# Kernel optimization log

Hardware: AMD Instinct MI355X
Metric: run time of the kernel (lower is better)

## Reference

```python
import jax, jax.numpy as jnp
import numpy as np

V, D, H_FF, NH, L = 32000, 1024, 4096, 16, 4
HD = D // NH  # 64
B, T = 2, 2048
EPS = 1e-6
ROPE_BASE = 10000.0


def setup_inputs() -> dict:
    key = jax.random.key(0)
    ks = jax.random.split(key, 16)
    s = 0.02
    inp = {
        "idx": jax.random.randint(ks[0], (B, T), 0, V, dtype=jnp.int32),
        "targets": jax.random.randint(ks[1], (B, T), 0, V, dtype=jnp.int32),
        "embed": jax.random.normal(ks[2], (V, D), jnp.float32) * s,
        "wq": jax.random.normal(ks[3], (L, D, D), jnp.float32) * s,
        "wk": jax.random.normal(ks[4], (L, D, D), jnp.float32) * s,
        "wv": jax.random.normal(ks[5], (L, D, D), jnp.float32) * s,
        "wo": jax.random.normal(ks[6], (L, D, D), jnp.float32) * s,
        "w_gate": jax.random.normal(ks[7], (L, D, H_FF), jnp.float32) * s,
        "w_up": jax.random.normal(ks[8], (L, D, H_FF), jnp.float32) * s,
        "w_down": jax.random.normal(ks[9], (L, H_FF, D), jnp.float32) * s,
        "attn_norm": jnp.ones((L, D), jnp.float32),
        "mlp_norm": jnp.ones((L, D), jnp.float32),
        "final_norm": jnp.ones((D,), jnp.float32),
        "lm_head": jax.random.normal(ks[10], (V, D), jnp.float32) * s,
    }
    return inp


def rms_norm(x, w):
    var = jnp.mean(jnp.square(x), axis=-1, keepdims=True)
    return x * jax.lax.rsqrt(var + EPS) * w


def make_rope(t_len, hd):
    inv_freq = 1.0 / (ROPE_BASE ** (jnp.arange(0, hd, 2, dtype=jnp.float32) / hd))
    angles = jnp.arange(t_len, dtype=jnp.float32)[:, None] * inv_freq[None, :]  # [T, HD/2]
    return jnp.cos(angles), jnp.sin(angles)


def apply_rope(x, cos, sin):
    # x: [B, T, NH, HD]; half-split rotation (HF Llama style)
    x1, x2 = jnp.split(x, 2, axis=-1)
    c = cos[None, :, None, :]
    s = sin[None, :, None, :]
    return jnp.concatenate([x1 * c - x2 * s, x2 * c + x1 * s], axis=-1)


def forward(idx, targets, embed, wq, wk, wv, wo, w_gate, w_up, w_down,
            attn_norm, mlp_norm, final_norm, lm_head):
    b, t_len = idx.shape
    x = embed[idx]  # [B, T, D]
    cos, sin = make_rope(t_len, HD)
    causal = jnp.tril(jnp.ones((t_len, t_len), dtype=bool))
    scale = 1.0 / np.sqrt(HD)
    for l in range(L):
        # attention
        h = rms_norm(x, attn_norm[l])
        q = (h @ wq[l]).reshape(b, t_len, NH, HD)
        k = (h @ wk[l]).reshape(b, t_len, NH, HD)
        v = (h @ wv[l]).reshape(b, t_len, NH, HD)
        q = apply_rope(q, cos, sin)
        k = apply_rope(k, cos, sin)
        scores = jnp.einsum('bqhd,bkhd->bhqk', q, k) * scale
        scores = jnp.where(causal[None, None], scores, -jnp.inf)
        attn = jax.nn.softmax(scores, axis=-1)
        o = jnp.einsum('bhqk,bkhd->bqhd', attn, v).reshape(b, t_len, D)
        x = x + o @ wo[l]
        # SwiGLU MLP
        h = rms_norm(x, mlp_norm[l])
        x = x + (jax.nn.silu(h @ w_gate[l]) * (h @ w_up[l])) @ w_down[l]
    x = rms_norm(x, final_norm)
    logits = jnp.einsum('btd,vd->btv', x, lm_head)  # [B, T, V]
    logp = jax.nn.log_softmax(logits, axis=-1)
    nll = -jnp.take_along_axis(logp, targets[..., None], axis=-1)[..., 0]
    loss = jnp.mean(nll)
    return logits, loss


def reference(idx, targets, embed, wq, wk, wv, wo, w_gate, w_up, w_down,
              attn_norm, mlp_norm, final_norm, lm_head):
    return forward(idx, targets, embed, wq, wk, wv, wo, w_gate, w_up, w_down,
                   attn_norm, mlp_norm, final_norm, lm_head)
```

## Files before the change

### kernel.cpp

```cpp
#include <hip/hip_runtime.h>

typedef __attribute__((ext_vector_type(8))) short short8;
typedef __attribute__((ext_vector_type(4))) float f32x4;
typedef __attribute__((ext_vector_type(8))) unsigned short u16x8;
typedef unsigned short u16;

#define V_SIZE 32000
#define D_MODEL 1024
#define HFF 4096
#define NHEAD 16
#define HDIM 64
#define NLAYER 4
#define BT 4096
#define TSEQ 2048
#define QKV_STRIDE 3072
#define GU_STRIDE 8192
#define QSCALE 0.18033688011112043f

__device__ __forceinline__ u16 f2bf(float f) {
  union { float f; unsigned u; } v; v.f = f;
  unsigned r = v.u + 0x7fffu + ((v.u >> 16) & 1u);
  return (u16)(r >> 16);
}
__device__ __forceinline__ float bf2f(u16 h) {
  union { unsigned u; float f; } v; v.u = ((unsigned)h) << 16;
  return v.f;
}

__device__ __forceinline__ void gload_lds16(const void* g, void* l) {
  __builtin_amdgcn_global_load_lds((__attribute__((address_space(1))) void*)g,
                                   (__attribute__((address_space(3))) void*)l, 16, 0, 0);
}


__global__ void rope_table_kernel(float* __restrict__ cosb, float* __restrict__ sinb) {
  int i = blockIdx.x * 256 + threadIdx.x;
  int t = i >> 5, fi = i & 31;
  float freq = exp2f(-(2.0f * (float)fi / 64.0f) * log2f(10000.0f));
  float ang = (float)t * freq;
  cosb[i] = cosf(ang);
  sinb[i] = sinf(ang);
}

__global__ void convert_bf16_kernel(const float* __restrict__ src, u16* __restrict__ dst,
                                    const float* __restrict__ fn, long n8) {
  long i = (long)blockIdx.x * 256 + threadIdx.x;
  long stride = (long)gridDim.x * 256;
  for (; i < n8; i += stride) {
    const float4* s = (const float4*)(src + i * 8);
    float4 a = s[0], b = s[1];
    int k0 = (int)((i * 8) & (D_MODEL - 1));
    u16x8 r;
    r[0] = f2bf(a.x * fn[k0 + 0]); r[1] = f2bf(a.y * fn[k0 + 1]);
    r[2] = f2bf(a.z * fn[k0 + 2]); r[3] = f2bf(a.w * fn[k0 + 3]);
    r[4] = f2bf(b.x * fn[k0 + 4]); r[5] = f2bf(b.y * fn[k0 + 5]);
    r[6] = f2bf(b.z * fn[k0 + 6]); r[7] = f2bf(b.w * fn[k0 + 7]);
    *(u16x8*)(dst + i * 8) = r;
  }
}

__global__ __launch_bounds__(256) void transpose_bf16_kernel(const float* __restrict__ src0,
                                                             u16* __restrict__ dst0, int R, int C,
                                                             long srcStride, long dstStride,
                                                             int rowMode,
                                                             const float* __restrict__ nw0,
                                                             int nwStride) {
  __shared__ float tile[32][33];
  const float* src = src0 + (size_t)blockIdx.z * srcStride;
  u16* dst = dst0 + (size_t)blockIdx.z * dstStride;
  const float* nw = nw0 ? nw0 + (size_t)blockIdx.z * nwStride : nullptr;
  int tx = threadIdx.x & 31, ty = threadIdx.x >> 5;
  int bx = blockIdx.x, by = blockIdx.y;
#pragma unroll
  for (int i = 0; i < 32; i += 8) {
    int r = by * 32 + ty + i, c = bx * 32 + tx;
    tile[ty + i][tx] = src[(size_t)r * C + c];
  }
  __syncthreads();
#pragma unroll
  for (int i = 0; i < 32; i += 8) {
    int c = bx * 32 + ty + i;
    int r = by * 32 + tx;
    float val = tile[tx][ty + i];
    if (nw) val *= nw[r];
    int drow = c;
    if (rowMode == 1) drow = ((c >> 6) << 7) | (c & 63);
    else if (rowMode == 2) drow = ((c >> 6) << 7) | 64 | (c & 63);
    dst[(size_t)drow * R + r] = f2bf(val);
  }
}

__global__ __launch_bounds__(256) void embed_gather_kernel(const int* __restrict__ idx,
                                                           const float* __restrict__ embed,
                                                           u16* __restrict__ xb,
                                                           float* __restrict__ rinv) {
  int t = blockIdx.x;
  int id = idx[t];
  float4 v = ((const float4*)embed)[(size_t)id * 256 + threadIdx.x];
  u16* hp = xb + (size_t)t * D_MODEL + threadIdx.x * 4;
  hp[0] = f2bf(v.x); hp[1] = f2bf(v.y); hp[2] = f2bf(v.z); hp[3] = f2bf(v.w);
  float ss = v.x * v.x + v.y * v.y + v.z * v.z + v.w * v.w;
#pragma unroll
  for (int m = 32; m > 0; m >>= 1) ss += __shfl_xor(ss, m, 64);
  __shared__ float wsum[4];
  if ((threadIdx.x & 63) == 0) wsum[threadIdx.x >> 6] = ss;
  __syncthreads();
  if (threadIdx.x == 0) {
    float tot = wsum[0] + wsum[1] + wsum[2] + wsum[3];
    rinv[t] = rsqrtf(tot * (1.0f / (float)D_MODEL) + 1e-6f);
  }
}

__global__ void rinv_kernel(const float* __restrict__ ssqPart, float* __restrict__ rinv) {
  int r = blockIdx.x * 256 + threadIdx.x;
  float s = 0.f;
#pragma unroll
  for (int i = 0; i < 16; i++) s += ssqPart[(size_t)r * 16 + i];
  rinv[r] = rsqrtf(s * (1.0f / (float)D_MODEL) + 1e-6f);
}

__global__ void scale_xb_kernel(const u16* __restrict__ xb, const float* __restrict__ rinv,
                                u16* __restrict__ xbf) {
  long i = (long)blockIdx.x * 256 + threadIdx.x;
  int row = (int)(i >> 7);
  float ri = rinv[row];
  short8 v = *(const short8*)(xb + i * 8);
  u16x8 r;
#pragma unroll
  for (int j = 0; j < 8; j++) r[j] = f2bf(bf2f((u16)v[j]) * ri);
  *(u16x8*)(xbf + i * 8) = r;
}

__global__ __launch_bounds__(256) void vtrans_kernel(const u16* __restrict__ qkv,
                                                     u16* __restrict__ vt) {
  __shared__ u16 lds[64 * 64];
  const int tid = threadIdx.x;
  const int bh = blockIdx.y, tt = blockIdx.x;
  const int b = bh >> 4, h = bh & 15;
  const int tok0 = b * TSEQ + tt * 64;
  const int hoff = 2 * D_MODEL + h * HDIM;
#pragma unroll
  for (int it = 0; it < 2; it++) {
    int idx = it * 256 + tid;
    int row = idx >> 3, c = (idx & 7) * 8;
    short8 v = *(const short8*)(qkv + (size_t)(tok0 + row) * QKV_STRIDE + hoff + c);
    *(short8*)&lds[row * 64 + (c ^ ((row & 7) << 3))] = v;
  }
  __syncthreads();
#pragma unroll
  for (int it = 0; it < 2; it++) {
    int idx = it * 256 + tid;
    int d = idx >> 3, t0 = (idx & 7) * 8;
    u16x8 pk;
#pragma unroll
    for (int j = 0; j < 8; j++) {
      int t = t0 + j;
      pk[j] = lds[t * 64 + (((d & ~7) ^ ((t & 7) << 3)) | (d & 7))];
    }
    *(u16x8*)(vt + ((size_t)bh * 64 + d) * TSEQ + tt * 64 + t0) = pk;
  }
}

template <int EPI>
__global__ __launch_bounds__(256, 4) void gemm128_kernel(const u16* __restrict__ A,
                                                         const u16* __restrict__ B, void* Cp,
                                                         float* __restrict__ partM,
                                                         float* __restrict__ partS,
                                                         const float* __restrict__ cosb,
                                                         const float* __restrict__ sinb,
                                                         const float* __restrict__ rinv,
                                                         int M, int N, int K, int chunkBn) {
  __shared__ __align__(16) u16 smem_ab[2][128 * 64];
  u16* As = smem_ab[0];
  u16* Bs = smem_ab[1];
  const int tid = threadIdx.x;
  const int lane = tid & 63, wid = tid >> 6;
  const int wr = wid >> 1, wc = wid & 1;
  const int q = lane >> 4, l15 = lane & 15;
  const int nbm = M >> 7;
  const int nbmx = nbm >> 3;
  const int cs = nbm * chunkBn;
  const int chunk = (int)blockIdx.x / cs;
  const int r0 = (int)blockIdx.x - chunk * cs;
  const int s2 = r0 >> 3;
  const int bm = (r0 & 7) * nbmx + (s2 % nbmx);
  const int bn = chunk * chunkBn + (s2 / nbmx);
  const size_t abase = (size_t)bm * 128 * K;
  const size_t bbase = (size_t)bn * 128 * K;
  f32x4 acc[4][4] = {};
  for (int k0 = 0; k0 < K; k0 += 64) {
#pragma unroll
    for (int i = 0; i < 4; i++) {
      int idx8 = i * 256 + tid;
      int row = idx8 >> 3, ch = idx8 & 7;
      int sc = (ch ^ (row & 7)) << 3;
      gload_lds16(A + abase + (size_t)row * K + k0 + sc, As + idx8 * 8);
      gload_lds16(B + bbase + (size_t)row * K + k0 + sc, Bs + idx8 * 8);
    }
    __syncthreads();
#pragma unroll
    for (int ks = 0; ks < 2; ks++) {
      short8 af[4], bfr[4];
      int chunkc = ks * 4 + q;
#pragma unroll
      for (int mi = 0; mi < 4; mi++) {
        int row = wr * 64 + mi * 16 + l15;
        af[mi] = *(const short8*)&As[row * 64 + ((chunkc ^ (row & 7)) << 3)];
      }
#pragma unroll
      for (int ni = 0; ni < 4; ni++) {
        int row = wc * 64 + ni * 16 + l15;
        bfr[ni] = *(const short8*)&Bs[row * 64 + ((chunkc ^ (row & 7)) << 3)];
      }
#pragma unroll
      for (int mi = 0; mi < 4; mi++)
#pragma unroll
        for (int ni = 0; ni < 4; ni++)
          acc[mi][ni] = __builtin_amdgcn_mfma_f32_16x16x32_bf16(af[mi], bfr[ni], acc[mi][ni], 0, 0, 0);
    }
    __syncthreads();
  }

  if (EPI == 5) {
    float* upf = (float*)&smem_ab[0][0];
    if (wc == 1) {
#pragma unroll
      for (int mi = 0; mi < 4; mi++)
#pragma unroll
        for (int ni = 0; ni < 4; ni++)
#pragma unroll
          for (int j = 0; j < 4; j++) {
            int r = wr * 64 + mi * 16 + q * 4 + j;
            int cswz = (ni ^ ((r >> 2) & 3)) * 16 + l15;
            upf[r * 64 + cswz] = acc[mi][ni][j];
          }
    }
    __syncthreads();
    if (wc == 0) {
#pragma unroll
      for (int mi = 0; mi < 4; mi++)
#pragma unroll
        for (int j = 0; j < 4; j++) {
          int rloc = wr * 64 + mi * 16 + q * 4 + j;
          int rr = bm * 128 + rloc;
          float ri = rinv[rr];
#pragma unroll
          for (int ni = 0; ni < 4; ni++) {
            int cswz = (ni ^ ((rloc >> 2) & 3)) * 16 + l15;
            float g = acc[mi][ni][j] * ri;
            float u = upf[rloc * 64 + cswz] * ri;
            float rsl = g / (1.0f + expf(-g)) * u;
            ((u16*)Cp)[(size_t)rr * (N >> 1) + bn * 64 + ni * 16 + l15] = f2bf(rsl);
          }
        }
    }
    return;
  }

#pragma unroll
  for (int mi = 0; mi < 4; mi++)
#pragma unroll
    for (int j = 0; j < 4; j++) {
      int rr = bm * 128 + wr * 64 + mi * 16 + q * 4 + j;
      float vv[4];
      if (EPI == 4) {
        float ri = rinv[rr];
        if (((bn << 1) + wc) < 16) ri *= QSCALE;
#pragma unroll
        for (int ni = 0; ni < 4; ni++) vv[ni] = acc[mi][ni][j] * ri;
      } else {
#pragma unroll
        for (int ni = 0; ni < 4; ni++) vv[ni] = acc[mi][ni][j];
      }
      if (EPI == 0) {
        float mx = fmaxf(fmaxf(vv[0], vv[1]), fmaxf(vv[2], vv[3]));
        mx = fmaxf(mx, __shfl_xor(mx, 1, 64));
        mx = fmaxf(mx, __shfl_xor(mx, 2, 64));
        mx = fmaxf(mx, __shfl_xor(mx, 4, 64));
        mx = fmaxf(mx, __shfl_xor(mx, 8, 64));
        float sm = 0.f;
#pragma unroll
        for (int ni = 0; ni < 4; ni++) sm += expf(vv[ni] - mx);
        sm += __shfl_xor(sm, 1, 64);
        sm += __shfl_xor(sm, 2, 64);
        sm += __shfl_xor(sm, 4, 64);
        sm += __shfl_xor(sm, 8, 64);
        if (l15 == 0) {
          int nt = (N >> 6);
          partM[(size_t)rr * nt + (bn << 1) + wc] = mx;
          partS[(size_t)rr * nt + (bn << 1) + wc] = sm;
        }
      }
      if (EPI == 4) {
        if (((bn << 1) + wc) < 32) {
          int t = rr & (TSEQ - 1);
#pragma unroll
          for (int ni = 0; ni < 2; ni++) {
            int fi = ni * 16 + l15;
            float c = cosb[t * 32 + fi], s = sinb[t * 32 + fi];
            float x1 = vv[ni], x2 = vv[ni + 2];
            vv[ni] = x1 * c - x2 * s;
            vv[ni + 2] = x2 * c + x1 * s;
          }
        }
      }
#pragma unroll
      for (int ni = 0; ni < 4; ni++) {
        int cn = bn * 128 + wc * 64 + ni * 16 + l15;
        size_t off = (size_t)rr * N + cn;
        if (EPI == 0) __builtin_nontemporal_store(vv[ni], (float*)Cp + off);
        else ((u16*)Cp)[off] = f2bf(vv[ni]);
      }
    }
}

__global__ __launch_bounds__(256, 4) void gemm64_kernel(const u16* __restrict__ A,
                                                        const u16* __restrict__ B,
                                                        const u16* __restrict__ resid,
                                                        u16* __restrict__ xbout,
                                                        float* __restrict__ ssqPart,
                                                        int M, int N, int K) {
  __shared__ __align__(16) u16 As[64 * 64];
  __shared__ __align__(16) u16 Bs[128 * 64];
  const int tid = threadIdx.x;
  const int lane = tid & 63, wid = tid >> 6;
  const int wr = wid >> 1, wc = wid & 1;
  const int q = lane >> 4, l15 = lane & 15;
  const int nbm = M >> 6;
  const int nbmx = nbm >> 3;
  const int s2 = (int)blockIdx.x >> 3;
  const int bm = ((int)blockIdx.x & 7) * nbmx + (s2 % nbmx);
  const int bn = s2 / nbmx;
  const size_t abase = (size_t)bm * 64 * K;
  const size_t bbase = (size_t)bn * 128 * K;
  f32x4 acc[2][4] = {};
  for (int k0 = 0; k0 < K; k0 += 64) {
#pragma unroll
    for (int i = 0; i < 2; i++) {
      int idx8 = i * 256 + tid;
      int row = idx8 >> 3, ch = idx8 & 7;
      int sc = (ch ^ (row & 7)) << 3;
      gload_lds16(A + abase + (size_t)row * K + k0 + sc, As + idx8 * 8);
    }
#pragma unroll
    for (int i = 0; i < 4; i++) {
      int idx8 = i * 256 + tid;
      int row = idx8 >> 3, ch = idx8 & 7;
      int sc = (ch ^ (row & 7)) << 3;
      gload_lds16(B + bbase + (size_t)row * K + k0 + sc, Bs + idx8 * 8);
    }
    __syncthreads();
#pragma unroll
    for (int ks = 0; ks < 2; ks++) {
      short8 af[2], bfr[4];
      int chunkc = ks * 4 + q;
#pragma unroll
      for (int mi = 0; mi < 2; mi++) {
        int row = wr * 32 + mi * 16 + l15;
        af[mi] = *(const short8*)&As[row * 64 + ((chunkc ^ (row & 7)) << 3)];
      }
#pragma unroll
      for (int ni = 0; ni < 4; ni++) {
        int row = wc * 64 + ni * 16 + l15;
        bfr[ni] = *(const short8*)&Bs[row * 64 + ((chunkc ^ (row & 7)) << 3)];
      }
#pragma unroll
      for (int mi = 0; mi < 2; mi++)
#pragma unroll
        for (int ni = 0; ni < 4; ni++)
          acc[mi][ni] = __builtin_amdgcn_mfma_f32_16x16x32_bf16(af[mi], bfr[ni], acc[mi][ni], 0, 0, 0);
    }
    __syncthreads();
  }
#pragma unroll
  for (int mi = 0; mi < 2; mi++)
#pragma unroll
    for (int j = 0; j < 4; j++) {
      int rr = bm * 64 + wr * 32 + mi * 16 + q * 4 + j;
      float ssq = 0.f;
#pragma unroll
      for (int ni = 0; ni < 4; ni++) {
        int cn = bn * 128 + wc * 64 + ni * 16 + l15;
        size_t off = (size_t)rr * N + cn;
        float nx = bf2f(resid[off]) + acc[mi][ni][j];
        xbout[off] = f2bf(nx);
        ssq += nx * nx;
      }
      ssq += __shfl_xor(ssq, 1, 64);
      ssq += __shfl_xor(ssq, 2, 64);
      ssq += __shfl_xor(ssq, 4, 64);
      ssq += __shfl_xor(ssq, 8, 64);
      if (l15 == 0) ssqPart[(size_t)rr * 16 + (bn << 1) + wc] = ssq;
    }
}

__global__ __launch_bounds__(256) void attn_kernel(const u16* __restrict__ qkv,
                                                   const u16* __restrict__ vt,
                                                   u16* __restrict__ o) {
  __shared__ __align__(16) u16 Ks[64 * 64];
  __shared__ __align__(16) u16 Vt[64 * 64];
  __shared__ u16 Ps[4][16 * 64];
  const u16* q = qkv;
  const u16* k = qkv + D_MODEL;
  const int tid = threadIdx.x, lane = tid & 63, wid = tid >> 6;
  const int qg = lane >> 4, l15 = lane & 15;
  const int bh = blockIdx.y;
  const int b = bh >> 4, h = bh & 15;
  const int tok0 = b * TSEQ;
  const int hoff = h * HDIM;
  const u16* vtb = vt + (size_t)bh * 64 * TSEQ;

  for (int half = 0; half < 2; half++) {
    const int qt = half == 0 ? (int)blockIdx.x : 31 - (int)blockIdx.x;
    const int qrow0 = qt * 64 + wid * 16;

    short8 aq[2];
#pragma unroll
    for (int ks = 0; ks < 2; ks++) {
      int r = qrow0 + l15;
      int d = ks * 32 + qg * 8;
      aq[ks] = *(const short8*)(q + (size_t)(tok0 + r) * QKV_STRIDE + hoff + d);
    }
    f32x4 oacc[4] = {};
    float mrow[4], lrow[4];
#pragma unroll
    for (int j = 0; j < 4; j++) { mrow[j] = -1e30f; lrow[j] = 0.f; }

    const int nkt = qt + 1;
    for (int kt = 0; kt < nkt; kt++) {
      const int kv0 = kt * 64;
#pragma unroll
      for (int it = 0; it < 2; it++) {
        int idx = it * 256 + tid;
        int row = idx >> 3, ch = idx & 7;
        int sc = (ch ^ (row & 7)) << 3;
        gload_lds16(k + (size_t)(tok0 + kv0 + row) * QKV_STRIDE + hoff + sc, Ks + idx * 8);
        gload_lds16(vtb + (size_t)row * TSEQ + kv0 + sc, Vt + idx * 8);
      }
      __syncthreads();
      f32x4 sc[4] = {};
#pragma unroll
      for (int ks = 0; ks < 2; ks++) {
        short8 bk[4];
        int kcol = ks * 32 + qg * 8;
#pragma unroll
        for (int ni = 0; ni < 4; ni++) {
          int r = ni * 16 + l15;
          bk[ni] = *(const short8*)&Ks[r * 64 + (kcol ^ ((r & 7) << 3))];
        }
#pragma unroll
        for (int ni = 0; ni < 4; ni++)
          sc[ni] = __builtin_amdgcn_mfma_f32_16x16x32_bf16(aq[ks], bk[ni], sc[ni], 0, 0, 0);
      }
      float pm[4];
#pragma unroll
      for (int j = 0; j < 4; j++) pm[j] = -1e30f;
      if (kt == qt) {
#pragma unroll
        for (int ni = 0; ni < 4; ni++)
#pragma unroll
          for (int j = 0; j < 4; j++) {
            int rq = qrow0 + qg * 4 + j;
            int ck = kv0 + ni * 16 + l15;
            float s = sc[ni][j];
            if (ck > rq) s = -1e30f;
            sc[ni][j] = s;
            pm[j] = fmaxf(pm[j], s);
          }
      } else {
#pragma unroll
        for (int ni = 0; ni < 4; ni++)
#pragma unroll
          for (int j = 0; j < 4; j++) pm[j] = fmaxf(pm[j], sc[ni][j]);
      }
#pragma unroll
      for (int j = 0; j < 4; j++) {
        float t = pm[j];
        t = fmaxf(t, __shfl_xor(t, 1, 64));
        t = fmaxf(t, __shfl_xor(t, 2, 64));
        t = fmaxf(t, __shfl_xor(t, 4, 64));
        t = fmaxf(t, __shfl_xor(t, 8, 64));
        pm[j] = t;
      }
#pragma unroll
      for (int j = 0; j < 4; j++) {
        float mn = fmaxf(mrow[j], pm[j]);
        float fac = exp2f(mrow[j] - mn);
        lrow[j] *= fac;
#pragma unroll
        for (int df = 0; df < 4; df++) oacc[df][j] *= fac;
        mrow[j] = mn;
      }
      float psum[4] = {};
#pragma unroll
      for (int ni = 0; ni < 4; ni++)
#pragma unroll
        for (int j = 0; j < 4; j++) {
          float p = exp2f(sc[ni][j] - mrow[j]);
          psum[j] += p;
          int r16 = qg * 4 + j;
          int cc = ni * 16 + l15;
          Ps[wid][r16 * 64 + (cc ^ ((r16 & 7) << 3))] = f2bf(p);
        }
#pragma unroll
      for (int j = 0; j < 4; j++) {
        float t = psum[j];
        t += __shfl_xor(t, 1, 64);
        t += __shfl_xor(t, 2, 64);
        t += __shfl_xor(t, 4, 64);
        t += __shfl_xor(t, 8, 64);
        lrow[j] += t;
      }
#pragma unroll
      for (int kf = 0; kf < 2; kf++) {
        short8 pa, bv[4];
        int kcol = kf * 32 + qg * 8;
        {
          int r = l15;
          pa = *(const short8*)&Ps[wid][r * 64 + (kcol ^ ((r & 7) << 3))];
        }
#pragma unroll
        for (int df = 0; df < 4; df++) {
          int r = df * 16 + l15;
          bv[df] = *(const short8*)&Vt[r * 64 + (kcol ^ ((r & 7) << 3))];
        }
#pragma unroll
        for (int df = 0; df < 4; df++)
          oacc[df] = __builtin_amdgcn_mfma_f32_16x16x32_bf16(pa, bv[df], oacc[df], 0, 0, 0);
      }
      __syncthreads();
    }
#pragma unroll
    for (int df = 0; df < 4; df++)
#pragma unroll
      for (int j = 0; j < 4; j++) {
        int r = qrow0 + qg * 4 + j;
        int d = df * 16 + l15;
        float val = oacc[df][j] / lrow[j];
        o[(size_t)(tok0 + r) * D_MODEL + hoff + d] = f2bf(val);
      }
  }
}


__global__ void nll_finalize_kernel(const float* __restrict__ partM, const float* __restrict__ partS,
                                    const float* __restrict__ logits, const int* __restrict__ targets,
                                    float* __restrict__ nll) {
  int tok = blockIdx.x;
  int lane = threadIdx.x;
  const int NTL = V_SIZE >> 6;
  float m = -1e30f, s = 0.f;
  for (int i = lane; i < NTL; i += 64) {
    float m2 = partM[(size_t)tok * NTL + i];
    float s2 = partS[(size_t)tok * NTL + i];
    float nm = fmaxf(m, m2);
    s = s * expf(m - nm) + s2 * expf(m2 - nm);
    m = nm;
  }
#pragma unroll
  for (int mask = 1; mask < 64; mask <<= 1) {
    float m2 = __shfl_xor(m, mask, 64);
    float s2 = __shfl_xor(s, mask, 64);
    float nm = fmaxf(m, m2);
    s = s * expf(m - nm) + s2 * expf(m2 - nm);
    m = nm;
  }
  if (lane == 0)
    nll[tok] = m + logf(s) - logits[(size_t)tok * V_SIZE + targets[tok]];
}

__global__ void loss_reduce_kernel(const float* __restrict__ nll, float* __restrict__ out) {
  float s = 0.f;
  for (int i = threadIdx.x; i < BT; i += 256) s += nll[i];
#pragma unroll
  for (int mask = 1; mask < 64; mask <<= 1) s += __shfl_xor(s, mask, 64);
  __shared__ float sm[4];
  if ((threadIdx.x & 63) == 0) sm[threadIdx.x >> 6] = s;
  __syncthreads();
  if (threadIdx.x == 0) out[0] = (sm[0] + sm[1] + sm[2] + sm[3]) / (float)BT;
}


extern "C" void kernel_launch(void* const* d_in, const int* in_sizes, int n_in,
                              void* d_out, int out_size, void* d_ws, size_t ws_size,
                              hipStream_t stream) {
  const int* idx = (const int*)d_in[0];
  const int* targets = (const int*)d_in[1];
  const float* embed = (const float*)d_in[2];
  const float* wq = (const float*)d_in[3];
  const float* wk = (const float*)d_in[4];
  const float* wv = (const float*)d_in[5];
  const float* wo = (const float*)d_in[6];
  const float* w_gate = (const float*)d_in[7];
  const float* w_up = (const float*)d_in[8];
  const float* w_down = (const float*)d_in[9];
  const float* attn_norm = (const float*)d_in[10];
  const float* mlp_norm = (const float*)d_in[11];
  const float* final_norm = (const float*)d_in[12];
  const float* lm_head = (const float*)d_in[13];
  float* out = (float*)d_out;

  char* ws = (char*)d_ws;
  size_t off = 0;
  auto alloc = [&](size_t bytes) {
    void* p = ws + off;
    off += (bytes + 255) & ~(size_t)255;
    return p;
  };
  const size_t DD = (size_t)D_MODEL * D_MODEL;
  float* rope_cos = (float*)alloc((size_t)TSEQ * 32 * 4);
  float* rope_sin = (float*)alloc((size_t)TSEQ * 32 * 4);
  u16* Xb = (u16*)alloc((size_t)BT * D_MODEL * 2);
  u16* XbF = (u16*)alloc((size_t)BT * D_MODEL * 2);
  float* Rinv = (float*)alloc((size_t)BT * 4);
  float* SsqP = (float*)alloc((size_t)BT * 16 * 4);
  u16* QKVb = (u16*)alloc((size_t)BT * QKV_STRIDE * 2);
  u16* Vtb = (u16*)alloc((size_t)32 * 64 * TSEQ * 2);
  u16* Ob = (u16*)alloc((size_t)BT * D_MODEL * 2);
  u16* Gb = (u16*)alloc((size_t)BT * HFF * 2);
  u16* WQKVT = (u16*)alloc((size_t)NLAYER * QKV_STRIDE * D_MODEL * 2);
  u16* WOT = (u16*)alloc((size_t)NLAYER * DD * 2);
  u16* WGU = (u16*)alloc((size_t)NLAYER * GU_STRIDE * D_MODEL * 2);
  u16* WDT = (u16*)alloc((size_t)NLAYER * D_MODEL * HFF * 2);
  u16* LMH = (u16*)alloc((size_t)V_SIZE * D_MODEL * 2);
  float* NLLb = (float*)alloc((size_t)BT * 4);
  float* PartM = (float*)alloc((size_t)BT * (V_SIZE >> 6) * 4);
  float* PartS = (float*)alloc((size_t)BT * (V_SIZE >> 6) * 4);

  rope_table_kernel<<<256, 256, 0, stream>>>(rope_cos, rope_sin);
  convert_bf16_kernel<<<4096, 256, 0, stream>>>(lm_head, LMH, final_norm, (long)V_SIZE * D_MODEL / 8);
  embed_gather_kernel<<<BT, 256, 0, stream>>>(idx, embed, Xb, Rinv);

  const long QKVW = (long)QKV_STRIDE * D_MODEL;
  const long GUW = (long)GU_STRIDE * D_MODEL;
  const long DW = (long)D_MODEL * HFF;
  transpose_bf16_kernel<<<dim3(32, 32, NLAYER), 256, 0, stream>>>(wq, WQKVT, D_MODEL, D_MODEL, DD, QKVW, 0, attn_norm, D_MODEL);
  transpose_bf16_kernel<<<dim3(32, 32, NLAYER), 256, 0, stream>>>(wk, WQKVT + DD, D_MODEL, D_MODEL, DD, QKVW, 0, attn_norm, D_MODEL);
  transpose_bf16_kernel<<<dim3(32, 32, NLAYER), 256, 0, stream>>>(wv, WQKVT + 2 * DD, D_MODEL, D_MODEL, DD, QKVW, 0, attn_norm, D_MODEL);
  transpose_bf16_kernel<<<dim3(32, 32, NLAYER), 256, 0, stream>>>(wo, WOT, D_MODEL, D_MODEL, DD, DD, 0, nullptr, 0);
  transpose_bf16_kernel<<<dim3(128, 32, NLAYER), 256, 0, stream>>>(w_gate, WGU, D_MODEL, HFF, DW, GUW, 1, mlp_norm, D_MODEL);
  transpose_bf16_kernel<<<dim3(128, 32, NLAYER), 256, 0, stream>>>(w_up, WGU, D_MODEL, HFF, DW, GUW, 2, mlp_norm, D_MODEL);
  transpose_bf16_kernel<<<dim3(32, 128, NLAYER), 256, 0, stream>>>(w_down, WDT, HFF, D_MODEL, DW, DW, 0, nullptr, 0);

  for (int l = 0; l < NLAYER; l++) {
    gemm128_kernel<4><<<(QKV_STRIDE / 128) * (BT / 128), 256, 0, stream>>>(
        Xb, WQKVT + (size_t)l * QKVW, QKVb, nullptr, nullptr, rope_cos, rope_sin,
        Rinv, BT, QKV_STRIDE, D_MODEL, QKV_STRIDE / 128);
    vtrans_kernel<<<dim3(32, 32), 256, 0, stream>>>(QKVb, Vtb);
    attn_kernel<<<dim3(16, 32), 256, 0, stream>>>(QKVb, Vtb, Ob);
    gemm64_kernel<<<(BT / 64) * (D_MODEL / 128), 256, 0, stream>>>(
        Ob, WOT + (size_t)l * DD, Xb, Xb, SsqP, BT, D_MODEL, D_MODEL);
    rinv_kernel<<<BT / 256, 256, 0, stream>>>(SsqP, Rinv);

    gemm128_kernel<5><<<(GU_STRIDE / 128) * (BT / 128), 256, 0, stream>>>(
        Xb, WGU + (size_t)l * GUW, Gb, nullptr, nullptr, nullptr, nullptr,
        Rinv, BT, GU_STRIDE, D_MODEL, 32);
    gemm64_kernel<<<(BT / 64) * (D_MODEL / 128), 256, 0, stream>>>(
        Gb, WDT + (size_t)l * DW, Xb, Xb, SsqP, BT, D_MODEL, HFF);
    rinv_kernel<<<BT / 256, 256, 0, stream>>>(SsqP, Rinv);
  }

  scale_xb_kernel<<<BT * D_MODEL / (256 * 8), 256, 0, stream>>>(Xb, Rinv, XbF);
  gemm128_kernel<0><<<(V_SIZE / 128) * (BT / 128), 256, 0, stream>>>(
      XbF, LMH, out, PartM, PartS, nullptr, nullptr,
      nullptr, BT, V_SIZE, D_MODEL, 50);
  nll_finalize_kernel<<<BT, 64, 0, stream>>>(PartM, PartS, out, targets, NLLb);
  loss_reduce_kernel<<<1, 256, 0, stream>>>(NLLb, out + (size_t)BT * V_SIZE);
}
```

Baseline: 1.649 ms.

## Double-buffer LDS in gemm64 and attention; interleave gate/up columns at 16 granularity

The gemm64 and attention kernels now double-buffer their LDS tiles, issuing global-to-LDS loads for the next K/V tile before computing on the current one, and synchronise with explicit vmcnt waits and barriers. Both declare occupancy 2 to make room for the larger shared memory. The gate/up weight interleave changes from 64-column to 16-column blocks, so the SwiGLU epilogue pairs gate and up accumulators inside each wave's registers. This removes the LDS round trip and barrier, and half the waves no longer sit idle in that epilogue. The cost is doubled LDS per block and possibly lower occupancy in the pipelined kernels.

```diff
diff --git a/kernel.cpp b/kernel.cpp
--- a/kernel.cpp
+++ b/kernel.cpp
@@ -84,8 +84,8 @@
     float val = tile[tx][ty + i];
     if (nw) val *= nw[r];
     int drow = c;
-    if (rowMode == 1) drow = ((c >> 6) << 7) | (c & 63);
-    else if (rowMode == 2) drow = ((c >> 6) << 7) | 64 | (c & 63);
+    if (rowMode == 1) drow = ((c >> 4) << 5) | (c & 15);
+    else if (rowMode == 2) drow = ((c >> 4) << 5) | 16 | (c & 15);
     dst[(size_t)drow * R + r] = f2bf(val);
   }
 }
@@ -170,9 +170,8 @@
                                                          const float* __restrict__ sinb,
                                                          const float* __restrict__ rinv,
                                                          int M, int N, int K, int chunkBn) {
-  __shared__ __align__(16) u16 smem_ab[2][128 * 64];
-  u16* As = smem_ab[0];
-  u16* Bs = smem_ab[1];
+  __shared__ __align__(16) u16 As[128 * 64];
+  __shared__ __align__(16) u16 Bs[128 * 64];
   const int tid = threadIdx.x;
   const int lane = tid & 63, wid = tid >> 6;
   const int wr = wid >> 1, wc = wid & 1;
@@ -222,38 +221,21 @@
   }
 
   if (EPI == 5) {
-    float* upf = (float*)&smem_ab[0][0];
-    if (wc == 1) {
-#pragma unroll
-      for (int mi = 0; mi < 4; mi++)
-#pragma unroll
-        for (int ni = 0; ni < 4; ni++)
-#pragma unroll
-          for (int j = 0; j < 4; j++) {
-            int r = wr * 64 + mi * 16 + q * 4 + j;
-            int cswz = (ni ^ ((r >> 2) & 3)) * 16 + l15;
-            upf[r * 64 + cswz] = acc[mi][ni][j];
-          }
-    }
-    __syncthreads();
-    if (wc == 0) {
-#pragma unroll
-      for (int mi = 0; mi < 4; mi++)
-#pragma unroll
-        for (int j = 0; j < 4; j++) {
-          int rloc = wr * 64 + mi * 16 + q * 4 + j;
-          int rr = bm * 128 + rloc;
-          float ri = rinv[rr];
-#pragma unroll
-          for (int ni = 0; ni < 4; ni++) {
-            int cswz = (ni ^ ((rloc >> 2) & 3)) * 16 + l15;
-            float g = acc[mi][ni][j] * ri;
-            float u = upf[rloc * 64 + cswz] * ri;
-            float rsl = g / (1.0f + expf(-g)) * u;
-            ((u16*)Cp)[(size_t)rr * (N >> 1) + bn * 64 + ni * 16 + l15] = f2bf(rsl);
-          }
+#pragma unroll
+    for (int mi = 0; mi < 4; mi++)
+#pragma unroll
+      for (int j = 0; j < 4; j++) {
+        int rr = bm * 128 + wr * 64 + mi * 16 + q * 4 + j;
+        float ri = rinv[rr];
+#pragma unroll
+        for (int pr = 0; pr < 2; pr++) {
+          float g = acc[mi][pr * 2][j] * ri;
+          float u = acc[mi][pr * 2 + 1][j] * ri;
+          float rsl = g / (1.0f + expf(-g)) * u;
+          int cn = (bn * 4 + wc * 2 + pr) * 16 + l15;
+          ((u16*)Cp)[(size_t)rr * (N >> 1) + cn] = f2bf(rsl);
         }
-    }
+      }
     return;
   }
 
@@ -314,14 +296,14 @@
     }
 }
 
-__global__ __launch_bounds__(256, 4) void gemm64_kernel(const u16* __restrict__ A,
+__global__ __launch_bounds__(256, 2) void gemm64_kernel(const u16* __restrict__ A,
                                                         const u16* __restrict__ B,
                                                         const u16* __restrict__ resid,
                                                         u16* __restrict__ xbout,
                                                         float* __restrict__ ssqPart,
                                                         int M, int N, int K) {
-  __shared__ __align__(16) u16 As[64 * 64];
-  __shared__ __align__(16) u16 Bs[128 * 64];
+  __shared__ __align__(16) u16 As[2][64 * 64];
+  __shared__ __align__(16) u16 Bs[2][128 * 64];
   const int tid = threadIdx.x;
   const int lane = tid & 63, wid = tid >> 6;
   const int wr = wid >> 1, wc = wid & 1;
@@ -333,23 +315,36 @@
   const int bn = s2 / nbmx;
   const size_t abase = (size_t)bm * 64 * K;
   const size_t bbase = (size_t)bn * 128 * K;
-  f32x4 acc[2][4] = {};
-  for (int k0 = 0; k0 < K; k0 += 64) {
+
+  auto stage = [&](int t, int b) {
+    const int k0 = t << 6;
 #pragma unroll
     for (int i = 0; i < 2; i++) {
       int idx8 = i * 256 + tid;
       int row = idx8 >> 3, ch = idx8 & 7;
       int sc = (ch ^ (row & 7)) << 3;
-      gload_lds16(A + abase + (size_t)row * K + k0 + sc, As + idx8 * 8);
+      gload_lds16(A + abase + (size_t)row * K + k0 + sc, &As[b][idx8 * 8]);
     }
 #pragma unroll
     for (int i = 0; i < 4; i++) {
       int idx8 = i * 256 + tid;
       int row = idx8 >> 3, ch = idx8 & 7;
       int sc = (ch ^ (row & 7)) << 3;
-      gload_lds16(B + bbase + (size_t)row * K + k0 + sc, Bs + idx8 * 8);
-    }
-    __syncthreads();
+      gload_lds16(B + bbase + (size_t)row * K + k0 + sc, &Bs[b][idx8 * 8]);
+    }
+  };
+
+  f32x4 acc[2][4] = {};
+  const int NT = K >> 6;
+  stage(0, 0);
+  asm volatile("s_waitcnt vmcnt(0)" ::: "memory");
+  __builtin_amdgcn_s_barrier();
+  asm volatile("" ::: "memory");
+  int buf = 0;
+  for (int kt = 0; kt < NT; kt++) {
+    if (kt + 1 < NT) stage(kt + 1, buf ^ 1);
+    const u16* lA = &As[buf][0];
+    const u16* lB = &Bs[buf][0];
 #pragma unroll
     for (int ks = 0; ks < 2; ks++) {
       short8 af[2], bfr[4];
@@ -357,12 +352,12 @@
 #pragma unroll
       for (int mi = 0; mi < 2; mi++) {
         int row = wr * 32 + mi * 16 + l15;
-        af[mi] = *(const short8*)&As[row * 64 + ((chunkc ^ (row & 7)) << 3)];
+        af[mi] = *(const short8*)&lA[row * 64 + ((chunkc ^ (row & 7)) << 3)];
       }
 #pragma unroll
       for (int ni = 0; ni < 4; ni++) {
         int row = wc * 64 + ni * 16 + l15;
-        bfr[ni] = *(const short8*)&Bs[row * 64 + ((chunkc ^ (row & 7)) << 3)];
+        bfr[ni] = *(const short8*)&lB[row * 64 + ((chunkc ^ (row & 7)) << 3)];
       }
 #pragma unroll
       for (int mi = 0; mi < 2; mi++)
@@ -370,7 +365,10 @@
         for (int ni = 0; ni < 4; ni++)
           acc[mi][ni] = __builtin_amdgcn_mfma_f32_16x16x32_bf16(af[mi], bfr[ni], acc[mi][ni], 0, 0, 0);
     }
-    __syncthreads();
+    asm volatile("s_waitcnt vmcnt(0)" ::: "memory");
+    __builtin_amdgcn_s_barrier();
+    asm volatile("" ::: "memory");
+    buf ^= 1;
   }
 #pragma unroll
   for (int mi = 0; mi < 2; mi++)
@@ -394,11 +392,11 @@
     }
 }
 
-__global__ __launch_bounds__(256) void attn_kernel(const u16* __restrict__ qkv,
-                                                   const u16* __restrict__ vt,
-                                                   u16* __restrict__ o) {
-  __shared__ __align__(16) u16 Ks[64 * 64];
-  __shared__ __align__(16) u16 Vt[64 * 64];
+__global__ __launch_bounds__(256, 2) void attn_kernel(const u16* __restrict__ qkv,
+                                                      const u16* __restrict__ vt,
+                                                      u16* __restrict__ o) {
+  __shared__ __align__(16) u16 Ks[2][64 * 64];
+  __shared__ __align__(16) u16 Vt[2][64 * 64];
   __shared__ u16 Ps[4][16 * 64];
   const u16* q = qkv;
   const u16* k = qkv + D_MODEL;
@@ -410,6 +408,17 @@
   const int hoff = h * HDIM;
   const u16* vtb = vt + (size_t)bh * 64 * TSEQ;
 
+  auto stage = [&](int kv0, int bf) {
+#pragma unroll
+    for (int it = 0; it < 2; it++) {
+      int idx = it * 256 + tid;
+      int row = idx >> 3, ch = idx & 7;
+      int sc = (ch ^ (row & 7)) << 3;
+      gload_lds16(k + (size_t)(tok0 + kv0 + row) * QKV_STRIDE + hoff + sc, &Ks[bf][idx * 8]);
+      gload_lds16(vtb + (size_t)row * TSEQ + kv0 + sc, &Vt[bf][idx * 8]);
+    }
+  };
+
   for (int half = 0; half < 2; half++) {
     const int qt = half == 0 ? (int)blockIdx.x : 31 - (int)blockIdx.x;
     const int qrow0 = qt * 64 + wid * 16;
@@ -427,17 +436,16 @@
     for (int j = 0; j < 4; j++) { mrow[j] = -1e30f; lrow[j] = 0.f; }
 
     const int nkt = qt + 1;
+    stage(0, 0);
+    asm volatile("s_waitcnt vmcnt(0)" ::: "memory");
+    __builtin_amdgcn_s_barrier();
+    asm volatile("" ::: "memory");
+    int buf = 0;
     for (int kt = 0; kt < nkt; kt++) {
       const int kv0 = kt * 64;
-#pragma unroll
-      for (int it = 0; it < 2; it++) {
-        int idx = it * 256 + tid;
-        int row = idx >> 3, ch = idx & 7;
-        int sc = (ch ^ (row & 7)) << 3;
-        gload_lds16(k + (size_t)(tok0 + kv0 + row) * QKV_STRIDE + hoff + sc, Ks + idx * 8);
-        gload_lds16(vtb + (size_t)row * TSEQ + kv0 + sc, Vt + idx * 8);
-      }
-      __syncthreads();
+      if (kt + 1 < nkt) stage(kv0 + 64, buf ^ 1);
+      const u16* KsB = &Ks[buf][0];
+      const u16* VtB = &Vt[buf][0];
       f32x4 sc[4] = {};
 #pragma unroll
       for (int ks = 0; ks < 2; ks++) {
@@ -446,7 +454,7 @@
 #pragma unroll
         for (int ni = 0; ni < 4; ni++) {
           int r = ni * 16 + l15;
-          bk[ni] = *(const short8*)&Ks[r * 64 + (kcol ^ ((r & 7) << 3))];
+          bk[ni] = *(const short8*)&KsB[r * 64 + (kcol ^ ((r & 7) << 3))];
         }
 #pragma unroll
         for (int ni = 0; ni < 4; ni++)
@@ -522,13 +530,16 @@
 #pragma unroll
         for (int df = 0; df < 4; df++) {
           int r = df * 16 + l15;
-          bv[df] = *(const short8*)&Vt[r * 64 + (kcol ^ ((r & 7) << 3))];
+          bv[df] = *(const short8*)&VtB[r * 64 + (kcol ^ ((r & 7) << 3))];
         }
 #pragma unroll
         for (int df = 0; df < 4; df++)
           oacc[df] = __builtin_amdgcn_mfma_f32_16x16x32_bf16(pa, bv[df], oacc[df], 0, 0, 0);
       }
-      __syncthreads();
+      asm volatile("s_waitcnt vmcnt(0)" ::: "memory");
+      __builtin_amdgcn_s_barrier();
+      asm volatile("" ::: "memory");
+      buf ^= 1;
     }
 #pragma unroll
     for (int df = 0; df < 4; df++)
```

Result: faster. 1.613 ms (-2.2%).
